# Kernel tuning notes

Hardware: AMD Instinct MI355X
Metric: run time of the kernel (lower is better)

Reference implementation:

```python
import jax, jax.numpy as jnp
import numpy as np

B, T, E = 4, 2048, 1024
NH = 16
HS = E // NH  # 64


def setup_inputs() -> dict:
    key = jax.random.key(0)
    k1, k2, k3 = jax.random.split(key, 3)
    x = jax.random.normal(k1, (B, T, E), dtype=jnp.float32)
    # nn.Linear weights, stored as [in, out] so forward is x @ W
    W_attn = jax.random.normal(k2, (E, 3 * E), dtype=jnp.float32) * (1.0 / np.sqrt(E))
    W_proj = jax.random.normal(k3, (E, E), dtype=jnp.float32) * (1.0 / np.sqrt(E))
    return {"x": x, "W_attn": W_attn, "W_proj": W_proj}


def reference(x, W_attn, W_proj):
    b, t, e = x.shape
    # qkv projection; rearrange 'b t (a nh hs) -> a b nh t hs'
    qkv = x @ W_attn                                  # [b, t, 3e]
    qkv = qkv.reshape(b, t, 3, NH, HS)
    qkv = jnp.transpose(qkv, (2, 0, 3, 1, 4))          # [3, b, nh, t, hs]
    q, k, v = qkv[0], qkv[1], qkv[2]

    scale = 1.0 / np.sqrt(HS)
    # the blocked online-softmax loop in the original computes exactly
    # dense causal softmax attention
    scores = jnp.einsum('bhqd,bhkd->bhqk', q * scale, k)  # [b, nh, t, t]
    causal = jnp.tril(jnp.ones((t, t), dtype=bool))
    scores = jnp.where(causal, scores, -jnp.inf)
    p = jax.nn.softmax(scores, axis=-1)
    o = jnp.einsum('bhqk,bhkd->bhqd', p, v)            # [b, nh, t, hs]

    y = jnp.transpose(o, (0, 2, 1, 3)).reshape(b, t, e)  # 'b nh t hs -> b t (nh hs)'
    return y @ W_proj
```

## Files before the change

kernel.cpp:

```cpp
#include <hip/hip_runtime.h>
#include <hip/hip_bf16.h>
#include <cstdint>


typedef __attribute__((ext_vector_type(8))) short short8;
typedef __attribute__((ext_vector_type(4))) float f32x4;

__device__ __forceinline__ f32x4 mfma16(short8 a, short8 b, f32x4 c) {
  return __builtin_amdgcn_mfma_f32_16x16x32_bf16(a, b, c, 0, 0, 0);
}

__device__ __forceinline__ void gload16(const void* g, void* l) {
  __builtin_amdgcn_global_load_lds(
      (const __attribute__((address_space(1))) unsigned int*)g,
      (__attribute__((address_space(3))) unsigned int*)l, 16, 0, 0);
}

__device__ __forceinline__ unsigned short f2bf(float f) {
  unsigned u = __float_as_uint(f);
  u += 0x7fff + ((u >> 16) & 1);
  return (unsigned short)(u >> 16);
}

__device__ __forceinline__ float fexp2(float x) {
  float r;
  asm("v_exp_f32 %0, %1" : "=v"(r) : "v"(x));
  return r;
}

__device__ __forceinline__ unsigned cvtpk(float lo, float hi) {
  unsigned r;
  asm("v_cvt_pk_bf16_f32 %0, %1, %2" : "=v"(r) : "v"(lo), "v"(hi));
  return r;
}

__global__ void cvt_x_kernel(const float* __restrict__ in,
                             unsigned short* __restrict__ out, int n4) {
  int i = blockIdx.x * blockDim.x + threadIdx.x;
  if (i >= n4) return;
  float4 v = ((const float4*)in)[i];
  ushort4 o;
  o.x = f2bf(v.x); o.y = f2bf(v.y); o.z = f2bf(v.z); o.w = f2bf(v.w);
  ((ushort4*)out)[i] = o;
}

__global__ void transpose_cvt_kernel(const float* __restrict__ W,
                                     unsigned short* __restrict__ Wt,
                                     int K, int N, float qs, int nscale) {
  __shared__ float tile[32][33];
  int n0 = blockIdx.x * 32, k0 = blockIdx.y * 32;
  int tx = threadIdx.x, ty = threadIdx.y;
#pragma unroll
  for (int i = 0; i < 32; i += 8)
    tile[ty + i][tx] = W[(size_t)(k0 + ty + i) * N + n0 + tx];
  __syncthreads();
#pragma unroll
  for (int i = 0; i < 32; i += 8) {
    int n = n0 + ty + i;
    float v = tile[tx][ty + i];
    if (n < nscale) v *= qs;
    Wt[(size_t)n * K + k0 + tx] = f2bf(v);
  }
}

template <int OUTF32, int VT>
__global__ __launch_bounds__(256) void gemm_bt_kernel(
    const unsigned short* __restrict__ A, const unsigned short* __restrict__ Bt,
    void* __restrict__ C, unsigned short* __restrict__ Cv,
    int M, int N, int K, int ldc) {
  __shared__ __align__(16) unsigned short As[128 * 64];
  __shared__ __align__(16) unsigned short Bs[128 * 64];
  const int tid = threadIdx.x;
  const int lane = tid & 63;
  const int w = tid >> 6;
  const int wr = w >> 1, wc = w & 1;
  const int l15 = lane & 15, g = lane >> 4;
  const int m0 = blockIdx.x * 128, n0 = blockIdx.y * 128;

  f32x4 acc[4][4];
#pragma unroll
  for (int m = 0; m < 4; ++m)
#pragma unroll
    for (int n = 0; n < 4; ++n) acc[m][n] = (f32x4){0.f, 0.f, 0.f, 0.f};

  for (int k0 = 0; k0 < K; k0 += 64) {
    __syncthreads();
#pragma unroll
    for (int i = 0; i < 4; ++i) {
      int c = tid + 256 * i;
      int row = c >> 3;
      int piece = (c & 7) ^ (row & 7);
      gload16(A + (size_t)(m0 + row) * K + k0 + piece * 8, (char*)As + c * 16);
      gload16(Bt + (size_t)(n0 + row) * K + k0 + piece * 8, (char*)Bs + c * 16);
    }
    asm volatile("s_waitcnt vmcnt(0)" ::: "memory");
    __syncthreads();

#pragma unroll
    for (int kk = 0; kk < 2; ++kk) {
      short8 av[4], bv[4];
#pragma unroll
      for (int m = 0; m < 4; ++m) {
        int row = wr * 64 + m * 16 + l15;
        av[m] = *(const short8*)((const char*)As + row * 128 +
                                 ((kk * 64 + g * 16) ^ ((row & 7) << 4)));
      }
#pragma unroll
      for (int n = 0; n < 4; ++n) {
        int row = wc * 64 + n * 16 + l15;
        bv[n] = *(const short8*)((const char*)Bs + row * 128 +
                                 ((kk * 64 + g * 16) ^ ((row & 7) << 4)));
      }
#pragma unroll
      for (int m = 0; m < 4; ++m)
#pragma unroll
        for (int n = 0; n < 4; ++n)
          acc[m][n] = mfma16(av[m], bv[n], acc[m][n]);
    }
  }

  if (!VT || n0 < 2048) {
#pragma unroll
    for (int m = 0; m < 4; ++m)
#pragma unroll
      for (int n = 0; n < 4; ++n)
#pragma unroll
        for (int r = 0; r < 4; ++r) {
          size_t row = (size_t)(m0 + wr * 64 + m * 16 + g * 4 + r);
          size_t col = (size_t)(n0 + wc * 64 + n * 16 + l15);
          if (OUTF32)
            ((float*)C)[row * ldc + col] = acc[m][n][r];
          else
            ((unsigned short*)C)[row * ldc + col] = f2bf(acc[m][n][r]);
        }
  } else {
#pragma unroll
    for (int m = 0; m < 4; ++m)
#pragma unroll
      for (int n = 0; n < 4; ++n)
#pragma unroll
        for (int r = 0; r < 4; ++r) {
          int row = m0 + wr * 64 + m * 16 + g * 4 + r;
          int col = n0 + wc * 64 + n * 16 + l15 - 2048;
          int bb = row >> 11, t = row & 2047;
          size_t dst = ((size_t)(bb * 16 + (col >> 6)) * 64 + (col & 63)) * 2048 + t;
          Cv[dst] = f2bf(acc[m][n][r]);
        }
  }
}

__global__ __launch_bounds__(512, 4) void attn_kernel(
    const unsigned short* __restrict__ qk,
    const unsigned short* __restrict__ vt,
    unsigned short* __restrict__ o) {
  const int rb = blockIdx.x;
  const int xcd = rb & 7, slot = (rb >> 3) & 31, phase = rb >> 8;
  const int bh = xcd * 8 + (slot & 7);
  const int qtb = slot >> 3;
  const int qt = phase ? (7 - qtb) : qtb;
  const int b = bh >> 4, h = bh & 15;
  const int tid = threadIdx.x;
  const int w = tid >> 6, lane = tid & 63;
  const int l15 = lane & 15, g = lane >> 4;
  const int qb0 = qt * 256 + w * 32;

  __shared__ __align__(16) unsigned short Ks[2][64 * 64];
  __shared__ __align__(16) unsigned short Vs[2][64 * 64];
  __shared__ __align__(16) unsigned short Pl[8][32 * 64];
  char* pw = (char*)&Pl[w][0];

  const size_t row0 = (size_t)b * 2048;

  const int srow = tid >> 3;
  const int spiece = (tid & 7) ^ (srow & 7);
  const unsigned short* ksrc =
      qk + (row0 + srow) * 2048 + 1024 + h * 64 + spiece * 8;
  const unsigned short* vsrc =
      vt + ((size_t)bh * 64 + srow) * 2048 + spiece * 8;

  const int nt = 4 * qt + 4;

  gload16(ksrc, (char*)Ks[0] + tid * 16);
  gload16(vsrc, (char*)Vs[0] + tid * 16);

  short8 qf[2][2];
#pragma unroll
  for (int u = 0; u < 2; ++u) {
    const unsigned short* qp = qk + (row0 + qb0 + u * 16 + l15) * 2048 + h * 64;
#pragma unroll
    for (int c = 0; c < 2; ++c) qf[u][c] = *(const short8*)(qp + c * 32 + g * 8);
  }

  f32x4 acc[2][4];
#pragma unroll
  for (int u = 0; u < 2; ++u)
#pragma unroll
    for (int n = 0; n < 4; ++n) acc[u][n] = (f32x4){0.f, 0.f, 0.f, 0.f};
  float lsum[2] = {0.f, 0.f};

  for (int kt = 0; kt < nt; ++kt) {
    const int cur = kt & 1;
    asm volatile("s_waitcnt vmcnt(0)" ::: "memory");
    __syncthreads();
    if (kt + 1 < nt) {
      gload16(ksrc + (size_t)(kt + 1) * 64 * 2048,
              (char*)Ks[cur ^ 1] + tid * 16);
      gload16(vsrc + (kt + 1) * 64, (char*)Vs[cur ^ 1] + tid * 16);
    }

    const int ktb = kt * 64;
    if (ktb > qb0 + 31) continue;

    short8 kf[4][2];
#pragma unroll
    for (int tt = 0; tt < 4; ++tt) {
      int row = tt * 16 + l15;
      const char* base = (const char*)Ks[cur] + row * 128;
      int sw = (row & 7) << 4;
      kf[tt][0] = *(const short8*)(base + ((g * 16) ^ sw));
      kf[tt][1] = *(const short8*)(base + ((64 + g * 16) ^ sw));
    }

#pragma unroll
    for (int u = 0; u < 2; ++u) {
      f32x4 st[4];
#pragma unroll
      for (int tt = 0; tt < 4; ++tt) {
        st[tt] = mfma16(kf[tt][0], qf[u][0], (f32x4){0.f, 0.f, 0.f, 0.f});
        st[tt] = mfma16(kf[tt][1], qf[u][1], st[tt]);
      }
      const int qbu = qb0 + u * 16;
      const int prow = u * 16 + l15;
      const int psw = (prow & 7) << 4;
      char* pb = pw + prow * 128;
      float part = 0.f;
      if (ktb + 63 > qbu) {
        const int qq = qbu + l15;
#pragma unroll
        for (int tt = 0; tt < 4; ++tt) {
          float p4[4];
#pragma unroll
          for (int r4 = 0; r4 < 4; ++r4) {
            float s = st[tt][r4];
            if (ktb + tt * 16 + 4 * g + r4 > qq) s = -1e30f;
            float e = fexp2(s);
            part += e;
            p4[r4] = e;
          }
          uint2 pk;
          pk.x = cvtpk(p4[0], p4[1]);
          pk.y = cvtpk(p4[2], p4[3]);
          *(uint2*)(pb + ((tt * 32 + g * 8) ^ psw)) = pk;
        }
      } else {
#pragma unroll
        for (int tt = 0; tt < 4; ++tt) {
          float p4[4];
#pragma unroll
          for (int r4 = 0; r4 < 4; ++r4) {
            float e = fexp2(st[tt][r4]);
            part += e;
            p4[r4] = e;
          }
          uint2 pk;
          pk.x = cvtpk(p4[0], p4[1]);
          pk.y = cvtpk(p4[2], p4[3]);
          *(uint2*)(pb + ((tt * 32 + g * 8) ^ psw)) = pk;
        }
      }
      lsum[u] += part;
    }

#pragma unroll
    for (int c2 = 0; c2 < 2; ++c2) {
      short8 vf[4];
#pragma unroll
      for (int n = 0; n < 4; ++n) {
        int row = n * 16 + l15;
        vf[n] = *(const short8*)((const char*)Vs[cur] + row * 128 +
                                 ((c2 * 64 + g * 16) ^ ((row & 7) << 4)));
      }
#pragma unroll
      for (int u = 0; u < 2; ++u) {
        int prow = u * 16 + l15;
        short8 pf = *(const short8*)(pw + prow * 128 +
                                     ((c2 * 64 + g * 16) ^ ((prow & 7) << 4)));
#pragma unroll
        for (int n = 0; n < 4; ++n) acc[u][n] = mfma16(pf, vf[n], acc[u][n]);
      }
    }
  }

#pragma unroll
  for (int u = 0; u < 2; ++u) {
    float l = lsum[u];
    l += __shfl_xor(l, 16);
    l += __shfl_xor(l, 32);
    float linv[4];
#pragma unroll
    for (int r = 0; r < 4; ++r)
      linv[r] = 1.f / __shfl(l, (lane & 48) + g * 4 + r);
#pragma unroll
    for (int n = 0; n < 4; ++n)
#pragma unroll
      for (int r = 0; r < 4; ++r) {
        size_t row = row0 + qb0 + u * 16 + g * 4 + r;
        o[row * 1024 + h * 64 + n * 16 + l15] = f2bf(acc[u][n][r] * linv[r]);
      }
  }
}

extern "C" void kernel_launch(void* const* d_in, const int* in_sizes, int n_in,
                              void* d_out, int out_size, void* d_ws,
                              size_t ws_size, hipStream_t stream) {
  const float* x = (const float*)d_in[0];
  const float* W_attn = (const float*)d_in[1];
  const float* W_proj = (const float*)d_in[2];
  float* out = (float*)d_out;

  char* ws = (char*)d_ws;
  unsigned short* xb  = (unsigned short*)(ws);
  unsigned short* Wta = (unsigned short*)(ws + (16u << 20));
  unsigned short* Wtp = (unsigned short*)(ws + (22u << 20));
  unsigned short* qkb = (unsigned short*)(ws + (24u << 20));
  unsigned short* vtb = (unsigned short*)(ws + (56u << 20));

  cvt_x_kernel<<<8192, 256, 0, stream>>>(x, xb, 8192 * 1024 / 4);
  transpose_cvt_kernel<<<dim3(96, 32), dim3(32, 8), 0, stream>>>(
      W_attn, Wta, 1024, 3072, 0.1803368801f, 1024);
  transpose_cvt_kernel<<<dim3(32, 32), dim3(32, 8), 0, stream>>>(
      W_proj, Wtp, 1024, 1024, 1.0f, 0);
  gemm_bt_kernel<0, 1><<<dim3(64, 24), 256, 0, stream>>>(
      xb, Wta, qkb, vtb, 8192, 3072, 1024, 2048);
  attn_kernel<<<512, 512, 0, stream>>>(qkb, vtb, xb);
  gemm_bt_kernel<1, 0><<<dim3(64, 8), 256, 0, stream>>>(
      xb, Wtp, out, nullptr, 8192, 1024, 1024, 1024);
}
```

Before: 257.5 us.

## Make attention a persistent kernel with atomic work queue, longest tiles first

Attention now launches 768 persistent blocks of 256 threads. Each block pulls (query-tile, head) items from a per-XCD atomic counter, taking the heaviest causal tiles first, and query tiles shrink from 256 to 128 rows. The counters live in the output buffer and are reset by the first conversion kernel, before the final GEMM overwrites that buffer. The aim is better load balance across the triangular causal work. The cost is an atomic and a block barrier per item, and K/V tiles are now reused by only four warps instead of eight.

Measured after the change: 239.6 us. -7.0%, faster.

```diff
diff --git a/kernel.cpp b/kernel.cpp
--- a/kernel.cpp
+++ b/kernel.cpp
@@ -35,7 +35,9 @@
 }
 
 __global__ void cvt_x_kernel(const float* __restrict__ in,
-                             unsigned short* __restrict__ out, int n4) {
+                             unsigned short* __restrict__ out, int n4,
+                             unsigned* __restrict__ ctr) {
+  if (blockIdx.x == 0 && threadIdx.x < 8) ctr[threadIdx.x] = 0u;
   int i = blockIdx.x * blockDim.x + threadIdx.x;
   if (i >= n4) return;
   float4 v = ((const float4*)in)[i];
@@ -149,164 +151,181 @@
   }
 }
 
-__global__ __launch_bounds__(512, 4) void attn_kernel(
+__global__ __launch_bounds__(256, 3) void attn_kernel(
     const unsigned short* __restrict__ qk,
     const unsigned short* __restrict__ vt,
-    unsigned short* __restrict__ o) {
-  const int rb = blockIdx.x;
-  const int xcd = rb & 7, slot = (rb >> 3) & 31, phase = rb >> 8;
-  const int bh = xcd * 8 + (slot & 7);
-  const int qtb = slot >> 3;
-  const int qt = phase ? (7 - qtb) : qtb;
-  const int b = bh >> 4, h = bh & 15;
+    unsigned short* __restrict__ o,
+    unsigned* __restrict__ ctr) {
+  const int q = blockIdx.x & 7;
   const int tid = threadIdx.x;
   const int w = tid >> 6, lane = tid & 63;
   const int l15 = lane & 15, g = lane >> 4;
-  const int qb0 = qt * 256 + w * 32;
 
   __shared__ __align__(16) unsigned short Ks[2][64 * 64];
   __shared__ __align__(16) unsigned short Vs[2][64 * 64];
-  __shared__ __align__(16) unsigned short Pl[8][32 * 64];
+  __shared__ __align__(16) unsigned short Pl[4][32 * 64];
+  __shared__ unsigned item_s;
   char* pw = (char*)&Pl[w][0];
 
-  const size_t row0 = (size_t)b * 2048;
-
-  const int srow = tid >> 3;
-  const int spiece = (tid & 7) ^ (srow & 7);
-  const unsigned short* ksrc =
-      qk + (row0 + srow) * 2048 + 1024 + h * 64 + spiece * 8;
-  const unsigned short* vsrc =
-      vt + ((size_t)bh * 64 + srow) * 2048 + spiece * 8;
-
-  const int nt = 4 * qt + 4;
-
-  gload16(ksrc, (char*)Ks[0] + tid * 16);
-  gload16(vsrc, (char*)Vs[0] + tid * 16);
-
-  short8 qf[2][2];
-#pragma unroll
-  for (int u = 0; u < 2; ++u) {
-    const unsigned short* qp = qk + (row0 + qb0 + u * 16 + l15) * 2048 + h * 64;
-#pragma unroll
-    for (int c = 0; c < 2; ++c) qf[u][c] = *(const short8*)(qp + c * 32 + g * 8);
-  }
-
-  f32x4 acc[2][4];
-#pragma unroll
-  for (int u = 0; u < 2; ++u)
-#pragma unroll
-    for (int n = 0; n < 4; ++n) acc[u][n] = (f32x4){0.f, 0.f, 0.f, 0.f};
-  float lsum[2] = {0.f, 0.f};
-
-  for (int kt = 0; kt < nt; ++kt) {
-    const int cur = kt & 1;
-    asm volatile("s_waitcnt vmcnt(0)" ::: "memory");
+  for (;;) {
+    if (tid == 0) item_s = atomicAdd(&ctr[q], 1u);
     __syncthreads();
-    if (kt + 1 < nt) {
-      gload16(ksrc + (size_t)(kt + 1) * 64 * 2048,
-              (char*)Ks[cur ^ 1] + tid * 16);
-      gload16(vsrc + (kt + 1) * 64, (char*)Vs[cur ^ 1] + tid * 16);
-    }
-
-    const int ktb = kt * 64;
-    if (ktb > qb0 + 31) continue;
-
-    short8 kf[4][2];
-#pragma unroll
-    for (int tt = 0; tt < 4; ++tt) {
-      int row = tt * 16 + l15;
-      const char* base = (const char*)Ks[cur] + row * 128;
-      int sw = (row & 7) << 4;
-      kf[tt][0] = *(const short8*)(base + ((g * 16) ^ sw));
-      kf[tt][1] = *(const short8*)(base + ((64 + g * 16) ^ sw));
-    }
-
+    const unsigned j = item_s;
+    if (j >= 128u) break;
+    const int cq = 15 - (int)(j >> 3);
+    const int bh = q * 8 + (int)(j & 7u);
+    const int b = bh >> 4, h = bh & 15;
+    const size_t row0 = (size_t)b * 2048;
+    const int qb0 = cq * 128 + w * 32;
+    const int nt = 2 * cq + 2;
+
+#pragma unroll
+    for (int i = 0; i < 2; ++i) {
+      int cc = tid + 256 * i;
+      int row = cc >> 3;
+      int piece = (cc & 7) ^ (row & 7);
+      gload16(qk + (row0 + row) * 2048 + 1024 + h * 64 + piece * 8,
+              (char*)Ks[0] + cc * 16);
+      gload16(vt + ((size_t)bh * 64 + row) * 2048 + piece * 8,
+              (char*)Vs[0] + cc * 16);
+    }
+
+    short8 qf[2][2];
 #pragma unroll
     for (int u = 0; u < 2; ++u) {
-      f32x4 st[4];
+      const unsigned short* qp =
+          qk + (row0 + qb0 + u * 16 + l15) * 2048 + h * 64;
+#pragma unroll
+      for (int c = 0; c < 2; ++c)
+        qf[u][c] = *(const short8*)(qp + c * 32 + g * 8);
+    }
+
+    f32x4 acc[2][4];
+#pragma unroll
+    for (int u = 0; u < 2; ++u)
+#pragma unroll
+      for (int n = 0; n < 4; ++n) acc[u][n] = (f32x4){0.f, 0.f, 0.f, 0.f};
+    float lsum[2] = {0.f, 0.f};
+
+    for (int kt = 0; kt < nt; ++kt) {
+      const int cur = kt & 1;
+      asm volatile("s_waitcnt vmcnt(0)" ::: "memory");
+      __syncthreads();
+      if (kt + 1 < nt) {
+#pragma unroll
+        for (int i = 0; i < 2; ++i) {
+          int cc = tid + 256 * i;
+          int row = cc >> 3;
+          int piece = (cc & 7) ^ (row & 7);
+          gload16(qk + (row0 + (kt + 1) * 64 + row) * 2048 + 1024 + h * 64 +
+                      piece * 8,
+                  (char*)Ks[cur ^ 1] + cc * 16);
+          gload16(vt + ((size_t)bh * 64 + row) * 2048 + (kt + 1) * 64 +
+                      piece * 8,
+                  (char*)Vs[cur ^ 1] + cc * 16);
+        }
+      }
+
+      const int ktb = kt * 64;
+      if (ktb > qb0 + 31) continue;
+
+      short8 kf[4][2];
 #pragma unroll
       for (int tt = 0; tt < 4; ++tt) {
-        st[tt] = mfma16(kf[tt][0], qf[u][0], (f32x4){0.f, 0.f, 0.f, 0.f});
-        st[tt] = mfma16(kf[tt][1], qf[u][1], st[tt]);
-      }
-      const int qbu = qb0 + u * 16;
-      const int prow = u * 16 + l15;
-      const int psw = (prow & 7) << 4;
-      char* pb = pw + prow * 128;
-      float part = 0.f;
-      if (ktb + 63 > qbu) {
-        const int qq = qbu + l15;
+        int row = tt * 16 + l15;
+        const char* base = (const char*)Ks[cur] + row * 128;
+        int sw = (row & 7) << 4;
+        kf[tt][0] = *(const short8*)(base + ((g * 16) ^ sw));
+        kf[tt][1] = *(const short8*)(base + ((64 + g * 16) ^ sw));
+      }
+
+#pragma unroll
+      for (int u = 0; u < 2; ++u) {
+        f32x4 st[4];
 #pragma unroll
         for (int tt = 0; tt < 4; ++tt) {
-          float p4[4];
-#pragma unroll
-          for (int r4 = 0; r4 < 4; ++r4) {
-            float s = st[tt][r4];
-            if (ktb + tt * 16 + 4 * g + r4 > qq) s = -1e30f;
-            float e = fexp2(s);
-            part += e;
-            p4[r4] = e;
+          st[tt] = mfma16(kf[tt][0], qf[u][0], (f32x4){0.f, 0.f, 0.f, 0.f});
+          st[tt] = mfma16(kf[tt][1], qf[u][1], st[tt]);
+        }
+        const int qbu = qb0 + u * 16;
+        const int prow = u * 16 + l15;
+        const int psw = (prow & 7) << 4;
+        char* pb = pw + prow * 128;
+        float part = 0.f;
+        if (ktb + 63 > qbu) {
+          const int qq = qbu + l15;
+#pragma unroll
+          for (int tt = 0; tt < 4; ++tt) {
+            float p4[4];
+#pragma unroll
+            for (int r4 = 0; r4 < 4; ++r4) {
+              float s = st[tt][r4];
+              if (ktb + tt * 16 + 4 * g + r4 > qq) s = -1e30f;
+              float e = fexp2(s);
+              part += e;
+              p4[r4] = e;
+            }
+            uint2 pk;
+            pk.x = cvtpk(p4[0], p4[1]);
+            pk.y = cvtpk(p4[2], p4[3]);
+            *(uint2*)(pb + ((tt * 32 + g * 8) ^ psw)) = pk;
           }
-          uint2 pk;
-          pk.x = cvtpk(p4[0], p4[1]);
-          pk.y = cvtpk(p4[2], p4[3]);
-          *(uint2*)(pb + ((tt * 32 + g * 8) ^ psw)) = pk;
-        }
-      } else {
-#pragma unroll
-        for (int tt = 0; tt < 4; ++tt) {
-          float p4[4];
-#pragma unroll
-          for (int r4 = 0; r4 < 4; ++r4) {
-            float e = fexp2(st[tt][r4]);
-            part += e;
-            p4[r4] = e;
+        } else {
+#pragma unroll
+          for (int tt = 0; tt < 4; ++tt) {
+            float p4[4];
+#pragma unroll
+            for (int r4 = 0; r4 < 4; ++r4) {
+              float e = fexp2(st[tt][r4]);
+              part += e;
+              p4[r4] = e;
+            }
+            uint2 pk;
+            pk.x = cvtpk(p4[0], p4[1]);
+            pk.y = cvtpk(p4[2], p4[3]);
+            *(uint2*)(pb + ((tt * 32 + g * 8) ^ psw)) = pk;
           }
-          uint2 pk;
-          pk.x = cvtpk(p4[0], p4[1]);
-          pk.y = cvtpk(p4[2], p4[3]);
-          *(uint2*)(pb + ((tt * 32 + g * 8) ^ psw)) = pk;
-        }
-      }
-      lsum[u] += part;
-    }
-
-#pragma unroll
-    for (int c2 = 0; c2 < 2; ++c2) {
-      short8 vf[4];
-#pragma unroll
-      for (int n = 0; n < 4; ++n) {
-        int row = n * 16 + l15;
-        vf[n] = *(const short8*)((const char*)Vs[cur] + row * 128 +
-                                 ((c2 * 64 + g * 16) ^ ((row & 7) << 4)));
-      }
-#pragma unroll
-      for (int u = 0; u < 2; ++u) {
-        int prow = u * 16 + l15;
-        short8 pf = *(const short8*)(pw + prow * 128 +
-                                     ((c2 * 64 + g * 16) ^ ((prow & 7) << 4)));
-#pragma unroll
-        for (int n = 0; n < 4; ++n) acc[u][n] = mfma16(pf, vf[n], acc[u][n]);
-      }
-    }
-  }
-
-#pragma unroll
-  for (int u = 0; u < 2; ++u) {
-    float l = lsum[u];
-    l += __shfl_xor(l, 16);
-    l += __shfl_xor(l, 32);
-    float linv[4];
-#pragma unroll
-    for (int r = 0; r < 4; ++r)
-      linv[r] = 1.f / __shfl(l, (lane & 48) + g * 4 + r);
-#pragma unroll
-    for (int n = 0; n < 4; ++n)
-#pragma unroll
-      for (int r = 0; r < 4; ++r) {
-        size_t row = row0 + qb0 + u * 16 + g * 4 + r;
-        o[row * 1024 + h * 64 + n * 16 + l15] = f2bf(acc[u][n][r] * linv[r]);
-      }
+        }
+        lsum[u] += part;
+      }
+
+#pragma unroll
+      for (int c2 = 0; c2 < 2; ++c2) {
+        short8 vf[4];
+#pragma unroll
+        for (int n = 0; n < 4; ++n) {
+          int row = n * 16 + l15;
+          vf[n] = *(const short8*)((const char*)Vs[cur] + row * 128 +
+                                   ((c2 * 64 + g * 16) ^ ((row & 7) << 4)));
+        }
+#pragma unroll
+        for (int u = 0; u < 2; ++u) {
+          int prow = u * 16 + l15;
+          short8 pf = *(const short8*)(
+              pw + prow * 128 + ((c2 * 64 + g * 16) ^ ((prow & 7) << 4)));
+#pragma unroll
+          for (int n = 0; n < 4; ++n) acc[u][n] = mfma16(pf, vf[n], acc[u][n]);
+        }
+      }
+    }
+
+#pragma unroll
+    for (int u = 0; u < 2; ++u) {
+      float l = lsum[u];
+      l += __shfl_xor(l, 16);
+      l += __shfl_xor(l, 32);
+      float linv[4];
+#pragma unroll
+      for (int r = 0; r < 4; ++r)
+        linv[r] = 1.f / __shfl(l, (lane & 48) + g * 4 + r);
+#pragma unroll
+      for (int n = 0; n < 4; ++n)
+#pragma unroll
+        for (int r = 0; r < 4; ++r) {
+          size_t row = row0 + qb0 + u * 16 + g * 4 + r;
+          o[row * 1024 + h * 64 + n * 16 + l15] = f2bf(acc[u][n][r] * linv[r]);
+        }
+    }
   }
 }
 
@@ -324,15 +343,16 @@
   unsigned short* Wtp = (unsigned short*)(ws + (22u << 20));
   unsigned short* qkb = (unsigned short*)(ws + (24u << 20));
   unsigned short* vtb = (unsigned short*)(ws + (56u << 20));
-
-  cvt_x_kernel<<<8192, 256, 0, stream>>>(x, xb, 8192 * 1024 / 4);
+  unsigned* ctr = (unsigned*)d_out;
+
+  cvt_x_kernel<<<8192, 256, 0, stream>>>(x, xb, 8192 * 1024 / 4, ctr);
   transpose_cvt_kernel<<<dim3(96, 32), dim3(32, 8), 0, stream>>>(
       W_attn, Wta, 1024, 3072, 0.1803368801f, 1024);
   transpose_cvt_kernel<<<dim3(32, 32), dim3(32, 8), 0, stream>>>(
       W_proj, Wtp, 1024, 1024, 1.0f, 0);
   gemm_bt_kernel<0, 1><<<dim3(64, 24), 256, 0, stream>>>(
       xb, Wta, qkb, vtb, 8192, 3072, 1024, 2048);
-  attn_kernel<<<512, 512, 0, stream>>>(qkb, vtb, xb);
+  attn_kernel<<<768, 256, 0, stream>>>(qkb, vtb, xb, ctr);
   gemm_bt_kernel<1, 0><<<dim3(64, 8), 256, 0, stream>>>(
       xb, Wtp, out, nullptr, 8192, 1024, 1024, 1024);
 }
```
